# Kernel tuning notes

Hardware: AMD Instinct MI355X
Metric: run time of the kernel (lower is better)

Reference implementation:

```python
import jax, jax.numpy as jnp
import numpy as np

N_NODES = 50000
N_EDGES = 600000
D_IN, D_HID, D_OUT = 128, 256, 128


def setup_inputs() -> dict:
    key = jax.random.key(0)
    ks = jax.random.split(key, 8)
    x = jax.random.normal(ks[0], (N_NODES, D_IN), dtype=jnp.float32)
    edge_index = jax.random.randint(ks[1], (2, N_EDGES), 0, N_NODES, dtype=jnp.int64)
    # init_method='uniform' -> edge_weights initialized to ones
    edge_weights = jnp.ones((N_EDGES,), dtype=jnp.float32)
    def lin(k, din, dout):
        s = 1.0 / np.sqrt(din)
        return jax.random.uniform(k, (din, dout), jnp.float32, -s, s)
    W1 = lin(ks[2], D_IN, D_HID)
    b1 = jnp.zeros((D_HID,), jnp.float32)
    W2 = lin(ks[3], D_HID, D_HID)
    b2 = jnp.zeros((D_HID,), jnp.float32)
    W3 = lin(ks[4], D_HID, D_OUT)
    b3 = jnp.zeros((D_OUT,), jnp.float32)
    return {"x": x, "edge_index": edge_index, "edge_weights": edge_weights,
            "W1": W1, "b1": b1, "W2": W2, "b2": b2, "W3": W3, "b3": b3}


def reference(x, edge_index, edge_weights, W1, b1, W2, b2, W3, b3):
    N = x.shape[0]
    # learnable metric: softplus on raw edge weights
    ew = jax.nn.softplus(edge_weights)
    src, dst = edge_index[0], edge_index[1]
    # GCNConv default: add self-loops with weight 1.0
    loop = jnp.arange(N, dtype=edge_index.dtype)
    s = jnp.concatenate([src, loop])
    d = jnp.concatenate([dst, loop])
    w = jnp.concatenate([ew, jnp.ones((N,), ew.dtype)])
    # symmetric degree normalization (gcn_norm); identical edge_weight across layers
    deg = jax.ops.segment_sum(w, d, num_segments=N)
    dinv = jnp.where(deg > 0, jax.lax.rsqrt(deg), jnp.zeros_like(deg))
    norm = dinv[s] * w * dinv[d]  # [E+N]

    def gcn_conv(h, W, b):
        h = h @ W                              # [N, dout]
        msg = h[s] * norm[:, None]             # gather + scale: [E+N, dout]
        out = jax.ops.segment_sum(msg, d, num_segments=N)  # scatter-add
        return out + b

    h = jax.nn.relu(gcn_conv(x, W1, b1))   # dropout p=0.0 -> identity
    h = jax.nn.relu(gcn_conv(h, W2, b2))
    return gcn_conv(h, W3, b3)
```

## Files before the change

### kernel.cpp

```cpp
#include <hip/hip_runtime.h>
#include <hip/hip_fp16.h>
#include <math.h>

#define N_NODES 50000
#define N_EDGES 600000
#define D_IN    128
#define D_HID   256
#define D_OUT   128
#define NB_SCAN ((N_NODES + 255) / 256)

typedef unsigned short u16;
typedef __attribute__((ext_vector_type(8))) _Float16 f16x8;
typedef __attribute__((ext_vector_type(4))) float f32x4;

__device__ __forceinline__ u16 f2h(float x) {
    __half h = __float2half_rn(x);
    return *reinterpret_cast<u16*>(&h);
}
__device__ __forceinline__ float h2f(u16 h) {
    __half hh = *reinterpret_cast<__half*>(&h);
    return __half2float(hh);
}
__device__ __forceinline__ float2 h2f2(unsigned int raw) {
    __half2 h = *reinterpret_cast<__half2*>(&raw);
    return __half22float2(h);
}
__device__ __forceinline__ int bcast_i(int v, int l) {
    return __builtin_amdgcn_readlane(v, l);
}
__device__ __forceinline__ float bcast_f(float v, int l) {
    return __int_as_float(__builtin_amdgcn_readlane(__float_as_int(v), l));
}


__global__ void k_hist(const int* __restrict__ dst, const float* __restrict__ w,
                       float* __restrict__ ew, int* __restrict__ rank,
                       int* __restrict__ cnt) {
    int e = blockIdx.x * blockDim.x + threadIdx.x;
    if (e >= N_EDGES) return;
    float x = w[e];
    ew[e] = fmaxf(x, 0.f) + log1pf(expf(-fabsf(x)));
    rank[e] = atomicAdd(&cnt[dst[e]], 1);
}

__global__ void k_scan1(const int* __restrict__ cnt, int* __restrict__ rowptr,
                        int* __restrict__ bsum) {
    __shared__ int s[256];
    int b = blockIdx.x, t = threadIdx.x;
    int i = b * 256 + t;
    int v = (i < N_NODES) ? cnt[i] : 0;
    s[t] = v;
    __syncthreads();
    for (int off = 1; off < 256; off <<= 1) {
        int u = (t >= off) ? s[t - off] : 0;
        __syncthreads();
        s[t] += u;
        __syncthreads();
    }
    if (i < N_NODES) rowptr[i] = s[t] - v;
    if (t == 255) bsum[b] = s[255];
}

__global__ void k_scan2(const int* __restrict__ bsum, int* __restrict__ boff) {
    __shared__ int s[256];
    int t = threadIdx.x;
    int v = (t < NB_SCAN) ? bsum[t] : 0;
    s[t] = v;
    __syncthreads();
    for (int off = 1; off < 256; off <<= 1) {
        int u = (t >= off) ? s[t - off] : 0;
        __syncthreads();
        s[t] += u;
        __syncthreads();
    }
    if (t < NB_SCAN) boff[t] = s[t] - v;
    if (t == 255) boff[NB_SCAN] = s[255];
}

__global__ void k_scan3(int* __restrict__ rowptr, const int* __restrict__ boff) {
    int b = blockIdx.x, t = threadIdx.x;
    int i = b * 256 + t;
    if (i < N_NODES) rowptr[i] += boff[b];
    if (i == 0) rowptr[N_NODES] = boff[NB_SCAN];
}

__global__ void k_fill2(const int* __restrict__ src, const int* __restrict__ dst,
                        const float* __restrict__ ew, const int* __restrict__ rank,
                        const int* __restrict__ rowptr, int2* __restrict__ ecsr) {
    int e = blockIdx.x * blockDim.x + threadIdx.x;
    if (e >= N_EDGES) return;
    int pos = rowptr[dst[e]] + rank[e];
    ecsr[pos] = make_int2(src[e], __float_as_int(ew[e]));
}

__global__ void k_degdinv(const int* __restrict__ rowptr, const int2* __restrict__ ecsr,
                          float* __restrict__ dinv) {
    int n = blockIdx.x * blockDim.x + threadIdx.x;
    if (n >= N_NODES) return;
    int beg = rowptr[n], end = rowptr[n + 1];
    float s = 1.0f;
    for (int p = beg; p < end; p++) s += __int_as_float(ecsr[p].y);
    dinv[n] = rsqrtf(s);
}

__global__ void k_norm(const int* __restrict__ rowptr, const float* __restrict__ dinv,
                       int2* __restrict__ ecsr) {
    int n = blockIdx.x * blockDim.x + threadIdx.x;
    if (n >= N_NODES) return;
    int beg = rowptr[n], end = rowptr[n + 1];
    float dn = dinv[n];
    for (int p = beg; p < end; p++) {
        int2 r = ecsr[p];
        float w = dinv[r.x] * __int_as_float(r.y) * dn;
        ecsr[p] = make_int2(r.x, __float_as_int(w));
    }
}


#define WPREP_TOTAL 131072

__global__ void k_wprep(const float* __restrict__ W1, const float* __restrict__ W2,
                        const float* __restrict__ W3,
                        u16* __restrict__ B1, u16* __restrict__ B2, u16* __restrict__ B3) {
    int idx = blockIdx.x * blockDim.x + threadIdx.x;
    const float* W; u16* B; int K, N, base;
    if (idx < 32768)       { W = W1; B = B1; K = 128; N = 256; base = 0; }
    else if (idx < 98304)  { W = W2; B = B2; K = 256; N = 256; base = 32768; }
    else if (idx < 131072) { W = W3; B = B3; K = 256; N = 128; base = 98304; }
    else return;
    int p = idx - base;
    int n = p % N, k = p / N;
    float x = W[(size_t)k * N + n];
    u16 hi = f2h(x);
    u16 lo = f2h(x - h2f(hi));
    B[(size_t)n * (2 * K) + k] = hi;
    B[(size_t)n * (2 * K) + K + k] = lo;
}


template <int D, int INF, int OUTM, bool BIAS>
__global__ __launch_bounds__(256) void k_agg(const void* __restrict__ inv,
                                             const int* __restrict__ rowptr,
                                             const int2* __restrict__ ecsr,
                                             const float* __restrict__ dinv,
                                             const float* __restrict__ bias,
                                             void* __restrict__ outv) {
    int node = blockIdx.x * 4 + (threadIdx.x >> 6);
    int lane = threadIdx.x & 63;
    if (node >= N_NODES) return;
    float dn = dinv[node];
    float dd = dn * dn;
    int beg = rowptr[node], end = rowptr[node + 1];
    int deg = end - beg;
    int esrc = 0;
    float ewv = 0.f;
    if (lane < deg) {
        int2 t = ecsr[beg + lane];
        esrc = t.x;
        ewv = __int_as_float(t.y);
    }
    int dcap = (deg > 64) ? 64 : deg;

    if (D == 256) {
        const float* inf = (const float*)inv;
        const u16* inh = (const u16*)inv;
        float ax, ay, az, aw;
        if (INF == 0) {
            float4 sv = *(reinterpret_cast<const float4*>(inf + (size_t)node * D) + lane);
            ax = dd * sv.x; ay = dd * sv.y; az = dd * sv.z; aw = dd * sv.w;
        } else {
            uint2 raw = *reinterpret_cast<const uint2*>(inh + (size_t)node * D + lane * 4);
            float2 f01 = h2f2(raw.x), f23 = h2f2(raw.y);
            ax = dd * f01.x; ay = dd * f01.y; az = dd * f23.x; aw = dd * f23.y;
        }
        int j = 0;
        for (; j + 8 <= dcap; j += 8) {
            int si[8]; float wv[8];
            #pragma unroll
            for (int k = 0; k < 8; ++k) {
                si[k] = bcast_i(esrc, j + k);
                wv[k] = bcast_f(ewv, j + k);
            }
            if (INF == 0) {
                float4 r[8];
                #pragma unroll
                for (int k = 0; k < 8; ++k)
                    r[k] = *(reinterpret_cast<const float4*>(inf + (size_t)si[k] * D) + lane);
                #pragma unroll
                for (int k = 0; k < 8; ++k) {
                    ax += wv[k] * r[k].x; ay += wv[k] * r[k].y;
                    az += wv[k] * r[k].z; aw += wv[k] * r[k].w;
                }
            } else {
                uint2 q[8];
                #pragma unroll
                for (int k = 0; k < 8; ++k)
                    q[k] = *reinterpret_cast<const uint2*>(inh + (size_t)si[k] * D + lane * 4);
                #pragma unroll
                for (int k = 0; k < 8; ++k) {
                    float2 a = h2f2(q[k].x), b = h2f2(q[k].y);
                    ax += wv[k] * a.x; ay += wv[k] * a.y;
                    az += wv[k] * b.x; aw += wv[k] * b.y;
                }
            }
        }
        for (; j < dcap; ++j) {
            int s0 = bcast_i(esrc, j);
            float w0 = bcast_f(ewv, j);
            if (INF == 0) {
                float4 r0 = *(reinterpret_cast<const float4*>(inf + (size_t)s0 * D) + lane);
                ax += w0 * r0.x; ay += w0 * r0.y; az += w0 * r0.z; aw += w0 * r0.w;
            } else {
                uint2 q0 = *reinterpret_cast<const uint2*>(inh + (size_t)s0 * D + lane * 4);
                float2 a0 = h2f2(q0.x), b0 = h2f2(q0.y);
                ax += w0 * a0.x; ay += w0 * a0.y; az += w0 * b0.x; aw += w0 * b0.y;
            }
        }
        for (int p = beg + 64; p < end; ++p) {
            int2 e0 = ecsr[p];
            float w0 = __int_as_float(e0.y);
            if (INF == 0) {
                float4 r0 = *(reinterpret_cast<const float4*>(inf + (size_t)e0.x * D) + lane);
                ax += w0 * r0.x; ay += w0 * r0.y; az += w0 * r0.z; aw += w0 * r0.w;
            } else {
                uint2 q0 = *reinterpret_cast<const uint2*>(inh + (size_t)e0.x * D + lane * 4);
                float2 a0 = h2f2(q0.x), b0 = h2f2(q0.y);
                ax += w0 * a0.x; ay += w0 * a0.y; az += w0 * b0.x; aw += w0 * b0.y;
            }
        }
        if (OUTM == 0) {
            float* out = (float*)outv;
            if (BIAS) {
                float4 b = *(reinterpret_cast<const float4*>(bias) + lane);
                ax += b.x; ay += b.y; az += b.z; aw += b.w;
            }
            float4 res; res.x = ax; res.y = ay; res.z = az; res.w = aw;
            *(reinterpret_cast<float4*>(out + (size_t)node * D) + lane) = res;
        } else {
            u16* out = (u16*)outv;
            ushort4 hv;
            hv.x = f2h(ax); hv.y = f2h(ay); hv.z = f2h(az); hv.w = f2h(aw);
            *reinterpret_cast<ushort4*>(out + (size_t)node * D + lane * 4) = hv;
        }
    } else {
        const float* inf = (const float*)inv;
        const u16* inh = (const u16*)inv;
        float ax, ay;
        if (INF == 0) {
            float2 sv = *(reinterpret_cast<const float2*>(inf + (size_t)node * D) + lane);
            ax = dd * sv.x; ay = dd * sv.y;
        } else {
            unsigned int raw = *reinterpret_cast<const unsigned int*>(inh + (size_t)node * D + lane * 2);
            float2 f = h2f2(raw);
            ax = dd * f.x; ay = dd * f.y;
        }
        int j = 0;
        for (; j + 8 <= dcap; j += 8) {
            int si[8]; float wv[8];
            #pragma unroll
            for (int k = 0; k < 8; ++k) {
                si[k] = bcast_i(esrc, j + k);
                wv[k] = bcast_f(ewv, j + k);
            }
            if (INF == 0) {
                float2 r[8];
                #pragma unroll
                for (int k = 0; k < 8; ++k)
                    r[k] = *(reinterpret_cast<const float2*>(inf + (size_t)si[k] * D) + lane);
                #pragma unroll
                for (int k = 0; k < 8; ++k) {
                    ax += wv[k] * r[k].x; ay += wv[k] * r[k].y;
                }
            } else {
                unsigned int q[8];
                #pragma unroll
                for (int k = 0; k < 8; ++k)
                    q[k] = *reinterpret_cast<const unsigned int*>(inh + (size_t)si[k] * D + lane * 2);
                #pragma unroll
                for (int k = 0; k < 8; ++k) {
                    float2 f = h2f2(q[k]);
                    ax += wv[k] * f.x; ay += wv[k] * f.y;
                }
            }
        }
        for (; j < dcap; ++j) {
            int s0 = bcast_i(esrc, j);
            float w0 = bcast_f(ewv, j);
            if (INF == 0) {
                float2 r0 = *(reinterpret_cast<const float2*>(inf + (size_t)s0 * D) + lane);
                ax += w0 * r0.x; ay += w0 * r0.y;
            } else {
                unsigned int q0 = *reinterpret_cast<const unsigned int*>(inh + (size_t)s0 * D + lane * 2);
                float2 f0 = h2f2(q0);
                ax += w0 * f0.x; ay += w0 * f0.y;
            }
        }
        for (int p = beg + 64; p < end; ++p) {
            int2 e0 = ecsr[p];
            float w0 = __int_as_float(e0.y);
            if (INF == 0) {
                float2 r0 = *(reinterpret_cast<const float2*>(inf + (size_t)e0.x * D) + lane);
                ax += w0 * r0.x; ay += w0 * r0.y;
            } else {
                unsigned int q0 = *reinterpret_cast<const unsigned int*>(inh + (size_t)e0.x * D + lane * 2);
                float2 f0 = h2f2(q0);
                ax += w0 * f0.x; ay += w0 * f0.y;
            }
        }
        if (OUTM == 0) {
            float* out = (float*)outv;
            if (BIAS) {
                float2 b = *(reinterpret_cast<const float2*>(bias) + lane);
                ax += b.x; ay += b.y;
            }
            float2 res; res.x = ax; res.y = ay;
            *(reinterpret_cast<float2*>(out + (size_t)node * D) + lane) = res;
        } else {
            u16* out = (u16*)outv;
            ushort2 hv; hv.x = f2h(ax); hv.y = f2h(ay);
            *reinterpret_cast<ushort2*>(out + (size_t)node * D + lane * 2) = hv;
        }
    }
}


template <int OUT, bool BIAS, bool RELU>
__global__ __launch_bounds__(256) void k_gemm_h(const u16* __restrict__ Ap,
                                                const u16* __restrict__ Bp,
                                                const float* __restrict__ bias,
                                                void* __restrict__ Cv,
                                                int M, int K, int NN) {
    const int KP2 = 2 * K;
    __shared__ u16 As[8 * 544];
    __shared__ u16 Bs[2 * 8 * 544];
    int tid = threadIdx.x;
    int bm = blockIdx.y * 128;
    int bn = blockIdx.x * 128;
    int l = tid & 63;
    int w = tid >> 6;
    int wr = w >> 1, wc = w & 1;

    f32x4 zero = {0.f, 0.f, 0.f, 0.f};
    f32x4 acc[4][4];
    #pragma unroll
    for (int i = 0; i < 4; i++)
        #pragma unroll
        for (int j = 0; j < 4; j++) acc[i][j] = zero;

    for (int k0 = 0; k0 < K; k0 += 32) {
        #pragma unroll
        for (int q = 0; q < 2; q++) {
            int idx = tid + q * 256;
            int r = idx >> 2, o = idx & 3;
            int gr = bm + r;
            uint4 va = make_uint4(0u, 0u, 0u, 0u);
            if (gr < M)
                va = *reinterpret_cast<const uint4*>(Ap + (size_t)gr * K + k0 + o * 8);
            *reinterpret_cast<uint4*>(&As[(r >> 4) * 544 + o * 136 + (r & 15) * 8]) = va;
        }
        #pragma unroll
        for (int q = 0; q < 4; q++) {
            int idx = tid + q * 256;
            int r = idx >> 3, oct = idx & 7;
            int hf = oct >> 2, o = oct & 3;
            uint4 vb = *reinterpret_cast<const uint4*>(
                Bp + (size_t)(bn + r) * KP2 + hf * K + k0 + o * 8);
            *reinterpret_cast<uint4*>(
                &Bs[hf * 4352 + (r >> 4) * 544 + o * 136 + (r & 15) * 8]) = vb;
        }
        __syncthreads();
        int fro = (l >> 4) * 136 + (l & 15) * 8;
        f16x8 a[4], bh[4], bl[4];
        #pragma unroll
        for (int i = 0; i < 4; i++)
            a[i] = *reinterpret_cast<const f16x8*>(&As[(wr * 4 + i) * 544 + fro]);
        #pragma unroll
        for (int j = 0; j < 4; j++) {
            bh[j] = *reinterpret_cast<const f16x8*>(&Bs[(wc * 4 + j) * 544 + fro]);
            bl[j] = *reinterpret_cast<const f16x8*>(&Bs[4352 + (wc * 4 + j) * 544 + fro]);
        }
        #pragma unroll
        for (int i = 0; i < 4; i++)
            #pragma unroll
            for (int j = 0; j < 4; j++) {
                acc[i][j] = __builtin_amdgcn_mfma_f32_16x16x32_f16(a[i], bh[j], acc[i][j], 0, 0, 0);
                acc[i][j] = __builtin_amdgcn_mfma_f32_16x16x32_f16(a[i], bl[j], acc[i][j], 0, 0, 0);
            }
        __syncthreads();
    }

    int cl = l & 15;
    int rq = (l >> 4) * 4;
    float bv[4];
    #pragma unroll
    for (int j = 0; j < 4; j++) {
        int gc = bn + wc * 64 + j * 16 + cl;
        bv[j] = BIAS ? bias[gc] : 0.f;
    }
    #pragma unroll
    for (int i = 0; i < 4; i++) {
        #pragma unroll
        for (int r = 0; r < 4; r++) {
            int grow = bm + wr * 64 + i * 16 + rq + r;
            if (grow >= M) continue;
            #pragma unroll
            for (int j = 0; j < 4; j++) {
                int gc = bn + wc * 64 + j * 16 + cl;
                float v = acc[i][j][r];
                if (BIAS) v += bv[j];
                if (RELU) v = fmaxf(v, 0.f);
                if (OUT == 0) {
                    ((float*)Cv)[(size_t)grow * NN + gc] = v;
                } else {
                    ((u16*)Cv)[(size_t)grow * NN + gc] = f2h(v);
                }
            }
        }
    }
}


extern "C" void kernel_launch(void* const* d_in, const int* in_sizes, int n_in,
                              void* d_out, int out_size, void* d_ws, size_t ws_size,
                              hipStream_t stream) {
    const float* x   = (const float*)d_in[0];
    const int*   ei  = (const int*)d_in[1];
    const float* wts = (const float*)d_in[2];
    const float* W1  = (const float*)d_in[3];
    const float* b1  = (const float*)d_in[4];
    const float* W2  = (const float*)d_in[5];
    const float* b2  = (const float*)d_in[6];
    const float* W3  = (const float*)d_in[7];
    const float* b3  = (const float*)d_in[8];
    float* out = (float*)d_out;
    const int* src = ei;
    const int* dst = ei + N_EDGES;

    float* bufA   = (float*)d_ws;
    float* bufB   = bufA + (size_t)N_NODES * D_HID;
    float* ew     = bufB + (size_t)N_NODES * D_HID;
    float* dinv   = ew + N_EDGES;
    int*   cnt    = (int*)(dinv + N_NODES);
    int*   rank   = cnt + N_NODES;
    int*   rowptr = rank + N_EDGES;
    int2*  ecsr   = (int2*)(rowptr + (N_NODES + 2));
    u16*   Wb1    = (u16*)(ecsr + N_EDGES);
    u16*   Wb2    = Wb1 + 256 * 256;
    u16*   Wb3    = Wb2 + 256 * 512;
    int*   bsum   = (int*)(Wb3 + 128 * 512);
    int*   boff   = bsum + NB_SCAN;

    hipMemsetAsync(cnt, 0, sizeof(int) * N_NODES, stream);

    int ethreads = 256;
    int eblocks = (N_EDGES + ethreads - 1) / ethreads;
    int nblocks = (N_NODES + 255) / 256;
    k_hist<<<eblocks, ethreads, 0, stream>>>(dst, wts, ew, rank, cnt);
    k_scan1<<<NB_SCAN, 256, 0, stream>>>(cnt, rowptr, bsum);
    k_scan2<<<1, 256, 0, stream>>>(bsum, boff);
    k_scan3<<<NB_SCAN, 256, 0, stream>>>(rowptr, boff);
    k_fill2<<<eblocks, ethreads, 0, stream>>>(src, dst, ew, rank, rowptr, ecsr);
    k_degdinv<<<nblocks, 256, 0, stream>>>(rowptr, ecsr, dinv);
    k_norm<<<nblocks, 256, 0, stream>>>(rowptr, dinv, ecsr);
    k_wprep<<<(WPREP_TOTAL + 255) / 256, 256, 0, stream>>>(W1, W2, W3, Wb1, Wb2, Wb3);

    int aggBlocks = (N_NODES + 3) / 4;
    int gy = (N_NODES + 127) / 128;

    k_agg<128, 0, 1, false><<<aggBlocks, 256, 0, stream>>>(x, rowptr, ecsr, dinv, nullptr, bufA);
    {
        dim3 g(2, gy);
        k_gemm_h<1, true, true><<<g, 256, 0, stream>>>((const u16*)bufA, Wb1, b1, bufB,
                                                       N_NODES, D_IN, D_HID);
    }
    k_agg<256, 1, 1, false><<<aggBlocks, 256, 0, stream>>>(bufB, rowptr, ecsr, dinv, nullptr, bufA);
    {
        dim3 g(2, gy);
        k_gemm_h<1, true, true><<<g, 256, 0, stream>>>((const u16*)bufA, Wb2, b2, bufB,
                                                       N_NODES, D_HID, D_HID);
    }
    {
        dim3 g(1, gy);
        k_gemm_h<1, false, false><<<g, 256, 0, stream>>>((const u16*)bufB, Wb3, nullptr, bufA,
                                                         N_NODES, D_HID, D_OUT);
    }
    k_agg<128, 1, 0, true><<<aggBlocks, 256, 0, stream>>>(bufA, rowptr, ecsr, dinv, b3, out);
}
```

Before: 339.8 us.

## Fuse degree and norm computation into histogram and CSR fill; merge scan stages

Computes the weighted in-degree with float atomics during the histogram pass, folds the second and third scan kernels into one kernel that also writes dinv, and computes the final normalized edge weight directly in the CSR fill. This removes the separate per-node degree and normalization kernels, which walked the CSR serially per thread, and cuts the number of launches. The aggregation kernel also switches its edge loads and output stores to nontemporal variants. The float atomic sum makes the degree depend on summation order, and each scan block now redoes the small block-sum scan.

```diff
diff --git a/kernel.cpp b/kernel.cpp
--- a/kernel.cpp
+++ b/kernel.cpp
@@ -12,6 +12,11 @@
 typedef unsigned short u16;
 typedef __attribute__((ext_vector_type(8))) _Float16 f16x8;
 typedef __attribute__((ext_vector_type(4))) float f32x4;
+typedef __attribute__((ext_vector_type(2))) float f32x2v;
+typedef __attribute__((ext_vector_type(4))) float f32x4v;
+typedef __attribute__((ext_vector_type(2))) unsigned int u32x2v;
+typedef __attribute__((ext_vector_type(2))) u16 u16x2v;
+typedef __attribute__((ext_vector_type(4))) u16 u16x4v;
 
 __device__ __forceinline__ u16 f2h(float x) {
     __half h = __float2half_rn(x);
@@ -35,12 +40,15 @@
 
 __global__ void k_hist(const int* __restrict__ dst, const float* __restrict__ w,
                        float* __restrict__ ew, int* __restrict__ rank,
-                       int* __restrict__ cnt) {
+                       int* __restrict__ cnt, float* __restrict__ degf) {
     int e = blockIdx.x * blockDim.x + threadIdx.x;
     if (e >= N_EDGES) return;
     float x = w[e];
-    ew[e] = fmaxf(x, 0.f) + log1pf(expf(-fabsf(x)));
-    rank[e] = atomicAdd(&cnt[dst[e]], 1);
+    float sp = fmaxf(x, 0.f) + log1pf(expf(-fabsf(x)));
+    ew[e] = sp;
+    int d = dst[e];
+    rank[e] = atomicAdd(&cnt[d], 1);
+    atomicAdd(&degf[d], sp);
 }
 
 __global__ void k_scan1(const int* __restrict__ cnt, int* __restrict__ rowptr,
@@ -61,11 +69,14 @@
     if (t == 255) bsum[b] = s[255];
 }
 
-__global__ void k_scan2(const int* __restrict__ bsum, int* __restrict__ boff) {
+__global__ void k_scan23(const int* __restrict__ bsum, int* __restrict__ rowptr,
+                         const float* __restrict__ degf, float* __restrict__ dinv) {
     __shared__ int s[256];
-    int t = threadIdx.x;
+    __shared__ int orig[256];
+    int b = blockIdx.x, t = threadIdx.x;
     int v = (t < NB_SCAN) ? bsum[t] : 0;
     s[t] = v;
+    orig[t] = v;
     __syncthreads();
     for (int off = 1; off < 256; off <<= 1) {
         int u = (t >= off) ? s[t - off] : 0;
@@ -73,47 +84,25 @@
         s[t] += u;
         __syncthreads();
     }
-    if (t < NB_SCAN) boff[t] = s[t] - v;
-    if (t == 255) boff[NB_SCAN] = s[255];
-}
-
-__global__ void k_scan3(int* __restrict__ rowptr, const int* __restrict__ boff) {
-    int b = blockIdx.x, t = threadIdx.x;
+    int boffb = s[b] - orig[b];
     int i = b * 256 + t;
-    if (i < N_NODES) rowptr[i] += boff[b];
-    if (i == 0) rowptr[N_NODES] = boff[NB_SCAN];
+    if (i < N_NODES) {
+        rowptr[i] += boffb;
+        dinv[i] = rsqrtf(1.0f + degf[i]);
+    }
+    if (b == 0 && t == 0) rowptr[N_NODES] = s[NB_SCAN - 1];
 }
 
 __global__ void k_fill2(const int* __restrict__ src, const int* __restrict__ dst,
                         const float* __restrict__ ew, const int* __restrict__ rank,
-                        const int* __restrict__ rowptr, int2* __restrict__ ecsr) {
+                        const int* __restrict__ rowptr, const float* __restrict__ dinv,
+                        int2* __restrict__ ecsr) {
     int e = blockIdx.x * blockDim.x + threadIdx.x;
     if (e >= N_EDGES) return;
-    int pos = rowptr[dst[e]] + rank[e];
-    ecsr[pos] = make_int2(src[e], __float_as_int(ew[e]));
-}
-
-__global__ void k_degdinv(const int* __restrict__ rowptr, const int2* __restrict__ ecsr,
-                          float* __restrict__ dinv) {
-    int n = blockIdx.x * blockDim.x + threadIdx.x;
-    if (n >= N_NODES) return;
-    int beg = rowptr[n], end = rowptr[n + 1];
-    float s = 1.0f;
-    for (int p = beg; p < end; p++) s += __int_as_float(ecsr[p].y);
-    dinv[n] = rsqrtf(s);
-}
-
-__global__ void k_norm(const int* __restrict__ rowptr, const float* __restrict__ dinv,
-                       int2* __restrict__ ecsr) {
-    int n = blockIdx.x * blockDim.x + threadIdx.x;
-    if (n >= N_NODES) return;
-    int beg = rowptr[n], end = rowptr[n + 1];
-    float dn = dinv[n];
-    for (int p = beg; p < end; p++) {
-        int2 r = ecsr[p];
-        float w = dinv[r.x] * __int_as_float(r.y) * dn;
-        ecsr[p] = make_int2(r.x, __float_as_int(w));
-    }
+    int s = src[e], d = dst[e];
+    int pos = rowptr[d] + rank[e];
+    float wfin = dinv[s] * ew[e] * dinv[d];
+    ecsr[pos] = make_int2(s, __float_as_int(wfin));
 }
 
 
@@ -155,9 +144,10 @@
     int esrc = 0;
     float ewv = 0.f;
     if (lane < deg) {
-        int2 t = ecsr[beg + lane];
-        esrc = t.x;
-        ewv = __int_as_float(t.y);
+        u32x2v t = __builtin_nontemporal_load(
+            reinterpret_cast<const u32x2v*>(ecsr) + beg + lane);
+        esrc = (int)t.x;
+        ewv = __uint_as_float(t.y);
     }
     int dcap = (deg > 64) ? 64 : deg;
 
@@ -234,13 +224,14 @@
                 float4 b = *(reinterpret_cast<const float4*>(bias) + lane);
                 ax += b.x; ay += b.y; az += b.z; aw += b.w;
             }
-            float4 res; res.x = ax; res.y = ay; res.z = az; res.w = aw;
-            *(reinterpret_cast<float4*>(out + (size_t)node * D) + lane) = res;
+            f32x4v res = {ax, ay, az, aw};
+            __builtin_nontemporal_store(res,
+                reinterpret_cast<f32x4v*>(out + (size_t)node * D) + lane);
         } else {
             u16* out = (u16*)outv;
-            ushort4 hv;
-            hv.x = f2h(ax); hv.y = f2h(ay); hv.z = f2h(az); hv.w = f2h(aw);
-            *reinterpret_cast<ushort4*>(out + (size_t)node * D + lane * 4) = hv;
+            u16x4v hv = {f2h(ax), f2h(ay), f2h(az), f2h(aw)};
+            __builtin_nontemporal_store(hv,
+                reinterpret_cast<u16x4v*>(out + (size_t)node * D + lane * 4));
         }
     } else {
         const float* inf = (const float*)inv;
@@ -313,12 +304,14 @@
                 float2 b = *(reinterpret_cast<const float2*>(bias) + lane);
                 ax += b.x; ay += b.y;
             }
-            float2 res; res.x = ax; res.y = ay;
-            *(reinterpret_cast<float2*>(out + (size_t)node * D) + lane) = res;
+            f32x2v res = {ax, ay};
+            __builtin_nontemporal_store(res,
+                reinterpret_cast<f32x2v*>(out + (size_t)node * D) + lane);
         } else {
             u16* out = (u16*)outv;
-            ushort2 hv; hv.x = f2h(ax); hv.y = f2h(ay);
-            *reinterpret_cast<ushort2*>(out + (size_t)node * D + lane * 2) = hv;
+            u16x2v hv = {f2h(ax), f2h(ay)};
+            __builtin_nontemporal_store(hv,
+                reinterpret_cast<u16x2v*>(out + (size_t)node * D + lane * 2));
         }
     }
 }
@@ -448,20 +441,17 @@
     u16*   Wb2    = Wb1 + 256 * 256;
     u16*   Wb3    = Wb2 + 256 * 512;
     int*   bsum   = (int*)(Wb3 + 128 * 512);
-    int*   boff   = bsum + NB_SCAN;
-
-    hipMemsetAsync(cnt, 0, sizeof(int) * N_NODES, stream);
+    float* degf   = bufB;
+
+    (void)hipMemsetAsync(cnt, 0, sizeof(int) * N_NODES, stream);
+    (void)hipMemsetAsync(degf, 0, sizeof(float) * N_NODES, stream);
 
     int ethreads = 256;
     int eblocks = (N_EDGES + ethreads - 1) / ethreads;
-    int nblocks = (N_NODES + 255) / 256;
-    k_hist<<<eblocks, ethreads, 0, stream>>>(dst, wts, ew, rank, cnt);
+    k_hist<<<eblocks, ethreads, 0, stream>>>(dst, wts, ew, rank, cnt, degf);
     k_scan1<<<NB_SCAN, 256, 0, stream>>>(cnt, rowptr, bsum);
-    k_scan2<<<1, 256, 0, stream>>>(bsum, boff);
-    k_scan3<<<NB_SCAN, 256, 0, stream>>>(rowptr, boff);
-    k_fill2<<<eblocks, ethreads, 0, stream>>>(src, dst, ew, rank, rowptr, ecsr);
-    k_degdinv<<<nblocks, 256, 0, stream>>>(rowptr, ecsr, dinv);
-    k_norm<<<nblocks, 256, 0, stream>>>(rowptr, dinv, ecsr);
+    k_scan23<<<NB_SCAN, 256, 0, stream>>>(bsum, rowptr, degf, dinv);
+    k_fill2<<<eblocks, ethreads, 0, stream>>>(src, dst, ew, rank, rowptr, dinv, ecsr);
     k_wprep<<<(WPREP_TOTAL + 255) / 256, 256, 0, stream>>>(W1, W2, W3, Wb1, Wb2, Wb3);
 
     int aggBlocks = (N_NODES + 3) / 4;
```

Result: slower. 373.5 us (+9.9%).
